# Kernel tuning notes

Measured on AMD Instinct MI355X. Metric: run time of the kernel, lower is better.

## Reference

```python
import jax, jax.numpy as jnp
import numpy as np

N = 8192      # nodes
C = 128       # node_channels
E = 262144    # edges (avg degree 32)


def _glorot(key, shape):
    lim = 1.0 / np.sqrt(shape[0])
    return jax.random.uniform(key, shape, jnp.float32, -lim, lim)


def setup_inputs() -> dict:
    key = jax.random.key(0)
    ks = jax.random.split(key, 12)
    inp = {
        "x": jax.random.normal(ks[0], (N, C), jnp.float32),
        "edge_index": jax.random.randint(ks[1], (2, E), 0, N, dtype=jnp.int32).astype(jnp.int64),
        # edge encoder: two parallel GCNConv layers producing source/target embeddings
        "Ws": _glorot(ks[2], (C, C)), "bs": jnp.zeros((C,), jnp.float32),
        "Wt": _glorot(ks[3], (C, C)), "bt": jnp.zeros((C,), jnp.float32),
        # NodeModel GCNConv weights (layers used in forward: 1, 2, mu, 5, 6)
        "W1": _glorot(ks[4], (C, C)), "b1": jnp.zeros((C,), jnp.float32),
        "W2": _glorot(ks[5], (C, C)), "b2": jnp.zeros((C,), jnp.float32),
        "Wmu": _glorot(ks[6], (C, C)), "bmu": jnp.zeros((C,), jnp.float32),
        "W5": _glorot(ks[7], (C, C)), "b5": jnp.zeros((C,), jnp.float32),
        "W6": _glorot(ks[8], (C, C)), "b6": jnp.zeros((C,), jnp.float32),
    }
    return inp


def _gcn(x, W, b, src, dst, dis, n):
    """GCNConv: D^-1/2 (A + I) D^-1/2 X W + b, edge flow src -> dst."""
    h = x @ W                                    # [n, C]
    norm = dis[src] * dis[dst]                   # [E]
    agg = jax.ops.segment_sum(h[src] * norm[:, None], dst, num_segments=n)
    agg = agg + h * (dis * dis)[:, None]         # self-loop term
    return agg + b


def reference(x, edge_index, Ws, bs, Wt, bt, W1, b1, W2, b2, Wmu, bmu, W5, b5, W6, b6):
    src, dst = edge_index[0], edge_index[1]
    n = x.shape[0]
    # degree with self-loops (shared by all GCN layers, same graph)
    deg = jax.ops.segment_sum(jnp.ones((src.shape[0],), x.dtype), dst, num_segments=n) + 1.0
    dis = deg ** -0.5

    # edge encoder -> source/target embeddings, dense inner-product decoder (sigmoid=False)
    s = _gcn(x, Ws, bs, src, dst, dis, n)
    t = _gcn(x, Wt, bt, src, dst, dis, n)
    adj_pred = s @ t.T                           # [n, n]

    # NodeModel (eval mode: reparametrize returns mu; logstd branch is dead code)
    h = jax.nn.relu(_gcn(x, W1, b1, src, dst, dis, n))
    h = jax.nn.relu(_gcn(h, W2, b2, src, dst, dis, n))
    h = _gcn(h, Wmu, bmu, src, dst, dis, n)
    h = jax.nn.relu(_gcn(h, W5, b5, src, dst, dis, n))
    h = jax.nn.relu(_gcn(h, W6, b6, src, dst, dis, n))
    return adj_pred, h
```

## Files before the change

### kernel.cpp

```cpp
#include <hip/hip_runtime.h>
#include <hip/hip_bf16.h>

#define CCH 128

typedef __attribute__((ext_vector_type(8))) short s8v;
typedef __attribute__((ext_vector_type(4))) float f4v;

__device__ __forceinline__ unsigned short f2bf(float f){
  unsigned int u = __float_as_uint(f);
  u += 0x7fffu + ((u >> 16) & 1u);
  return (unsigned short)(u >> 16);
}

__global__ void k_deg(const int* __restrict__ dst, int* __restrict__ deg, int e){
  int i = blockIdx.x * blockDim.x + threadIdx.x;
  if (i < e) atomicAdd(&deg[dst[i]], 1);
}

__global__ void k_dis(const int* __restrict__ deg, float* __restrict__ dis, int n){
  int i = blockIdx.x * blockDim.x + threadIdx.x;
  if (i < n) dis[i] = rsqrtf((float)deg[i] + 1.0f);
}

__global__ void k_scan(const int* __restrict__ deg, int* __restrict__ row_ptr,
                       int* __restrict__ cursor, int n){
  __shared__ int part[1024];
  int t = threadIdx.x;
  int base = t * 8;
  int loc[8];
  int s = 0;
  #pragma unroll
  for (int i = 0; i < 8; ++i){ loc[i] = s; s += deg[base + i]; }
  part[t] = s;
  __syncthreads();
  for (int off = 1; off < 1024; off <<= 1){
    int v = (t >= off) ? part[t - off] : 0;
    __syncthreads();
    part[t] += v;
    __syncthreads();
  }
  int prev = t ? part[t - 1] : 0;
  #pragma unroll
  for (int i = 0; i < 8; ++i){
    int v = prev + loc[i];
    row_ptr[base + i] = v;
    cursor[base + i]  = v;
  }
  if (t == 0) row_ptr[n] = part[1023];
}

__global__ void k_scatter(const int* __restrict__ src, const int* __restrict__ dst,
                          int* __restrict__ cursor, int* __restrict__ csr_src, int e){
  int i = blockIdx.x * blockDim.x + threadIdx.x;
  if (i < e){
    int d = dst[i];
    int pos = atomicAdd(&cursor[d], 1);
    csr_src[pos] = src[i];
  }
}

__global__ __launch_bounds__(256) void k_agg(const float* __restrict__ h,
                                             const float* __restrict__ dis,
                                             const int* __restrict__ row_ptr,
                                             const int* __restrict__ csr_src,
                                             float* __restrict__ out, int n){
  int node = (blockIdx.x * blockDim.x + threadIdx.x) >> 6;
  int lane = threadIdx.x & 63;
  if (node >= n) return;
  const float2* h2 = (const float2*)h;
  int st = row_ptr[node], en = row_ptr[node + 1];
  float ax = 0.f, ay = 0.f;
  for (int e = st; e < en; ++e){
    int s = csr_src[e];
    float ds = dis[s];
    float2 v = h2[(size_t)s * 64 + lane];
    ax += v.x * ds; ay += v.y * ds;
  }
  float di = dis[node];
  float2 sv = h2[(size_t)node * 64 + lane];
  float2 o;
  o.x = ax * di + sv.x * di * di;
  o.y = ay * di + sv.y * di * di;
  ((float2*)out)[(size_t)node * 64 + lane] = o;
}

__global__ __launch_bounds__(256) void k_gemm(const float* __restrict__ A,
                                              const float* __restrict__ W,
                                              const float* __restrict__ bias,
                                              float* __restrict__ out, int relu){
  __shared__ float sW[CCH * CCH];
  __shared__ float sA[32 * CCH];
  int tid = threadIdx.x;
  const float4* W4 = (const float4*)W;
  float4* sW4 = (float4*)sW;
  #pragma unroll
  for (int i = 0; i < 16; ++i) sW4[tid + i * 256] = W4[tid + i * 256];
  int row0 = blockIdx.x * 32;
  const float4* A4 = (const float4*)(A + (size_t)row0 * CCH);
  float4* sA4 = (float4*)sA;
  #pragma unroll
  for (int i = 0; i < 4; ++i) sA4[tid + i * 256] = A4[tid + i * 256];
  __syncthreads();

  int r  = (tid >> 4) << 1;
  int c0 = (tid & 15) << 3;
  float acc0[8] = {0}, acc1[8] = {0};
  for (int k = 0; k < CCH; ++k){
    float a0 = sA[r * CCH + k], a1 = sA[(r + 1) * CCH + k];
    const float* wr = &sW[k * CCH + c0];
    #pragma unroll
    for (int j = 0; j < 8; ++j){
      float w = wr[j];
      acc0[j] += a0 * w;
      acc1[j] += a1 * w;
    }
  }
  size_t g0 = (size_t)(row0 + r) * CCH + c0;
  #pragma unroll
  for (int j = 0; j < 8; ++j){
    float v0 = acc0[j] + bias[c0 + j];
    float v1 = acc1[j] + bias[c0 + j];
    if (relu){ v0 = fmaxf(v0, 0.f); v1 = fmaxf(v1, 0.f); }
    out[g0 + j] = v0;
    out[g0 + CCH + j] = v1;
  }
}

__global__ void k_tobf16(const float4* __restrict__ a, const float4* __restrict__ b,
                         ushort4* __restrict__ ao, ushort4* __restrict__ bo, int total4){
  int i = blockIdx.x * blockDim.x + threadIdx.x;
  if (i < total4){
    float4 va = a[i];
    float4 vb = b[i];
    ushort4 oa = { f2bf(va.x), f2bf(va.y), f2bf(va.z), f2bf(va.w) };
    ushort4 ob = { f2bf(vb.x), f2bf(vb.y), f2bf(vb.z), f2bf(vb.w) };
    ao[i] = oa;
    bo[i] = ob;
  }
}

__global__ __launch_bounds__(256) void k_adj(const unsigned short* __restrict__ S,
                                             const unsigned short* __restrict__ T,
                                             float* __restrict__ out, int n){
  __shared__ unsigned short sS[128 * 128];
  __shared__ unsigned short sT[128 * 128];
  int tid = threadIdx.x;
  int ntile = n >> 7;
  int tm = blockIdx.x / ntile;
  int tn = blockIdx.x % ntile;

  #pragma unroll
  for (int i = 0; i < 8; ++i){
    int cidx = i * 256 + tid;
    int row = cidx >> 4;
    int o   = cidx & 15;
    int boff = (o * 16) ^ ((row & 7) << 4);
    s8v v = ((const s8v*)(S + (size_t)(tm * 128 + row) * CCH))[o];
    *(s8v*)((char*)sS + row * 256 + boff) = v;
    s8v w = ((const s8v*)(T + (size_t)(tn * 128 + row) * CCH))[o];
    *(s8v*)((char*)sT + row * 256 + boff) = w;
  }
  __syncthreads();

  int lane = tid & 63;
  int w = tid >> 6;
  int wm = (w >> 1) * 64;
  int wn = (w & 1) * 64;

  f4v zero = {0.f, 0.f, 0.f, 0.f};
  f4v acc[4][4];
  #pragma unroll
  for (int a = 0; a < 4; ++a)
    #pragma unroll
    for (int b = 0; b < 4; ++b) acc[a][b] = zero;

  #pragma unroll
  for (int ks = 0; ks < 4; ++ks){
    int boff = ks * 64 + (lane >> 4) * 16;
    s8v af[4], bf[4];
    #pragma unroll
    for (int mi = 0; mi < 4; ++mi){
      int row = wm + mi * 16 + (lane & 15);
      af[mi] = *(const s8v*)((const char*)sS + row * 256 + (boff ^ ((row & 7) << 4)));
    }
    #pragma unroll
    for (int ni = 0; ni < 4; ++ni){
      int row = wn + ni * 16 + (lane & 15);
      bf[ni] = *(const s8v*)((const char*)sT + row * 256 + (boff ^ ((row & 7) << 4)));
    }
    #pragma unroll
    for (int mi = 0; mi < 4; ++mi)
      #pragma unroll
      for (int ni = 0; ni < 4; ++ni)
        acc[mi][ni] = __builtin_amdgcn_mfma_f32_16x16x32_bf16(af[mi], bf[ni], acc[mi][ni], 0, 0, 0);
  }

  int rbase = tm * 128 + wm + (lane >> 4) * 4;
  int cbase = tn * 128 + wn + (lane & 15);
  #pragma unroll
  for (int mi = 0; mi < 4; ++mi)
    #pragma unroll
    for (int ni = 0; ni < 4; ++ni){
      int rr = rbase + mi * 16;
      int cc = cbase + ni * 16;
      #pragma unroll
      for (int r = 0; r < 4; ++r)
        out[(size_t)(rr + r) * n + cc] = acc[mi][ni][r];
    }
}

extern "C" void kernel_launch(void* const* d_in, const int* in_sizes, int n_in,
                              void* d_out, int out_size, void* d_ws, size_t ws_size,
                              hipStream_t stream) {
  const float* x  = (const float*)d_in[0];
  const int*   ei = (const int*)d_in[1];
  const int n = in_sizes[0] / CCH;
  const int e = in_sizes[1] / 2;
  const int* srcv = ei;
  const int* dstv = ei + e;
  const float *Ws  = (const float*)d_in[2],  *bs  = (const float*)d_in[3];
  const float *Wt  = (const float*)d_in[4],  *bt  = (const float*)d_in[5];
  const float *W1  = (const float*)d_in[6],  *b1  = (const float*)d_in[7];
  const float *W2  = (const float*)d_in[8],  *b2  = (const float*)d_in[9];
  const float *Wmu = (const float*)d_in[10], *bmu = (const float*)d_in[11];
  const float *W5  = (const float*)d_in[12], *b5  = (const float*)d_in[13];
  const float *W6  = (const float*)d_in[14], *b6  = (const float*)d_in[15];

  char* ws = (char*)d_ws;
  size_t off = 0;
  auto alloc = [&](size_t bytes) -> void* {
    void* p = ws + off;
    off += (bytes + 255) & ~(size_t)255;
    return p;
  };
  int*   deg     = (int*)alloc((size_t)n * 4);
  float* dis     = (float*)alloc((size_t)n * 4);
  int*   row_ptr = (int*)alloc((size_t)(n + 1) * 4);
  int*   cursor  = (int*)alloc((size_t)n * 4);
  int*   csr_src = (int*)alloc((size_t)e * 4);
  float* aggX    = (float*)alloc((size_t)n * CCH * 4);
  float* sbuf    = (float*)alloc((size_t)n * CCH * 4);
  float* tbuf    = (float*)alloc((size_t)n * CCH * 4);
  float* P       = (float*)alloc((size_t)n * CCH * 4);
  float* Q       = (float*)alloc((size_t)n * CCH * 4);
  unsigned short* sb = (unsigned short*)alloc((size_t)n * CCH * 2);
  unsigned short* tb = (unsigned short*)alloc((size_t)n * CCH * 2);

  float* adj  = (float*)d_out;
  float* hout = (float*)d_out + (size_t)n * n;

  hipMemsetAsync(deg, 0, (size_t)n * 4, stream);
  k_deg    <<<(e + 255) / 256, 256, 0, stream>>>(dstv, deg, e);
  k_dis    <<<(n + 255) / 256, 256, 0, stream>>>(deg, dis, n);
  k_scan   <<<1, 1024, 0, stream>>>(deg, row_ptr, cursor, n);
  k_scatter<<<(e + 255) / 256, 256, 0, stream>>>(srcv, dstv, cursor, csr_src, e);

  k_agg <<<n / 4, 256, 0, stream>>>(x, dis, row_ptr, csr_src, aggX, n);
  k_gemm<<<n / 32, 256, 0, stream>>>(aggX, Ws, bs, sbuf, 0);
  k_gemm<<<n / 32, 256, 0, stream>>>(aggX, Wt, bt, tbuf, 0);
  k_gemm<<<n / 32, 256, 0, stream>>>(aggX, W1, b1, Q, 1);
  k_agg <<<n / 4, 256, 0, stream>>>(Q, dis, row_ptr, csr_src, P, n);
  k_gemm<<<n / 32, 256, 0, stream>>>(P, W2, b2, Q, 1);
  k_agg <<<n / 4, 256, 0, stream>>>(Q, dis, row_ptr, csr_src, P, n);
  k_gemm<<<n / 32, 256, 0, stream>>>(P, Wmu, bmu, Q, 0);
  k_agg <<<n / 4, 256, 0, stream>>>(Q, dis, row_ptr, csr_src, P, n);
  k_gemm<<<n / 32, 256, 0, stream>>>(P, W5, b5, Q, 1);
  k_agg <<<n / 4, 256, 0, stream>>>(Q, dis, row_ptr, csr_src, P, n);
  k_gemm<<<n / 32, 256, 0, stream>>>(P, W6, b6, hout, 1);

  k_tobf16<<<((n * CCH / 4) + 255) / 256, 256, 0, stream>>>(
      (const float4*)sbuf, (const float4*)tbuf, (ushort4*)sb, (ushort4*)tb, n * CCH / 4);
  int nt = n / 128;
  k_adj<<<nt * nt, 256, 0, stream>>>(sb, tb, adj, n);
}
```

Measured before the change: 553.3 us.

## Fold GCN normalization into GEMM epilogues and unroll gather aggregation

Factors D^-1/2 out of the edge loop. Each layer's output is pre-scaled by dis in the GEMM epilogue (and x by a new fused dis/scale kernel), so aggregation becomes a plain gather-sum with no per-edge dis loads or multiplies. The aggregation loop is unrolled by 8 with independent accumulators to raise memory-level parallelism. The GEMM block is halved to 16 rows to get more blocks, and the adj kernel is launched earlier in the stream. The risk is extra rounding from the changed accumulation order, plus a GEMM with less register reuse.

```diff
diff --git a/kernel.cpp b/kernel.cpp
--- a/kernel.cpp
+++ b/kernel.cpp
@@ -17,9 +17,16 @@
   if (i < e) atomicAdd(&deg[dst[i]], 1);
 }
 
-__global__ void k_dis(const int* __restrict__ deg, float* __restrict__ dis, int n){
-  int i = blockIdx.x * blockDim.x + threadIdx.x;
-  if (i < n) dis[i] = rsqrtf((float)deg[i] + 1.0f);
+__global__ __launch_bounds__(256) void k_disscale(const int* __restrict__ deg,
+    const float* __restrict__ x, float* __restrict__ dis, float* __restrict__ g, int n){
+  int t = blockIdx.x * 256 + threadIdx.x;
+  int i = t >> 5, c = t & 31;
+  if (i >= n) return;
+  float di = rsqrtf((float)deg[i] + 1.0f);
+  if (c == 0) dis[i] = di;
+  float4 v = ((const float4*)x)[(size_t)i * 32 + c];
+  v.x *= di; v.y *= di; v.z *= di; v.w *= di;
+  ((float4*)g)[(size_t)i * 32 + c] = v;
 }
 
 __global__ void k_scan(const int* __restrict__ deg, int* __restrict__ row_ptr,
@@ -59,70 +66,84 @@
   }
 }
 
-__global__ __launch_bounds__(256) void k_agg(const float* __restrict__ h,
-                                             const float* __restrict__ dis,
-                                             const int* __restrict__ row_ptr,
-                                             const int* __restrict__ csr_src,
-                                             float* __restrict__ out, int n){
+__global__ __launch_bounds__(256) void k_agg(const float* __restrict__ g,
+    const int* __restrict__ row_ptr, const int* __restrict__ csr_src,
+    float* __restrict__ out, int n){
   int node = (blockIdx.x * blockDim.x + threadIdx.x) >> 6;
   int lane = threadIdx.x & 63;
   if (node >= n) return;
-  const float2* h2 = (const float2*)h;
+  node = __builtin_amdgcn_readfirstlane(node);
+  const float2* g2 = (const float2*)g;
   int st = row_ptr[node], en = row_ptr[node + 1];
-  float ax = 0.f, ay = 0.f;
-  for (int e = st; e < en; ++e){
+  float2 sv = g2[(size_t)node * 64 + lane];
+  float ax0 = sv.x, ay0 = sv.y;
+  float ax1 = 0.f, ay1 = 0.f, ax2 = 0.f, ay2 = 0.f, ax3 = 0.f, ay3 = 0.f;
+  float ax4 = 0.f, ay4 = 0.f, ax5 = 0.f, ay5 = 0.f, ax6 = 0.f, ay6 = 0.f;
+  float ax7 = 0.f, ay7 = 0.f;
+  int e = st;
+  for (; e + 8 <= en; e += 8){
+    int s0 = csr_src[e + 0], s1 = csr_src[e + 1], s2 = csr_src[e + 2], s3 = csr_src[e + 3];
+    int s4 = csr_src[e + 4], s5 = csr_src[e + 5], s6 = csr_src[e + 6], s7 = csr_src[e + 7];
+    float2 v0 = g2[(size_t)s0 * 64 + lane];
+    float2 v1 = g2[(size_t)s1 * 64 + lane];
+    float2 v2 = g2[(size_t)s2 * 64 + lane];
+    float2 v3 = g2[(size_t)s3 * 64 + lane];
+    float2 v4 = g2[(size_t)s4 * 64 + lane];
+    float2 v5 = g2[(size_t)s5 * 64 + lane];
+    float2 v6 = g2[(size_t)s6 * 64 + lane];
+    float2 v7 = g2[(size_t)s7 * 64 + lane];
+    ax0 += v0.x; ay0 += v0.y;  ax1 += v1.x; ay1 += v1.y;
+    ax2 += v2.x; ay2 += v2.y;  ax3 += v3.x; ay3 += v3.y;
+    ax4 += v4.x; ay4 += v4.y;  ax5 += v5.x; ay5 += v5.y;
+    ax6 += v6.x; ay6 += v6.y;  ax7 += v7.x; ay7 += v7.y;
+  }
+  for (; e < en; ++e){
     int s = csr_src[e];
-    float ds = dis[s];
-    float2 v = h2[(size_t)s * 64 + lane];
-    ax += v.x * ds; ay += v.y * ds;
-  }
-  float di = dis[node];
-  float2 sv = h2[(size_t)node * 64 + lane];
+    float2 v = g2[(size_t)s * 64 + lane];
+    ax0 += v.x; ay0 += v.y;
+  }
   float2 o;
-  o.x = ax * di + sv.x * di * di;
-  o.y = ay * di + sv.y * di * di;
+  o.x = ((ax0 + ax1) + (ax2 + ax3)) + ((ax4 + ax5) + (ax6 + ax7));
+  o.y = ((ay0 + ay1) + (ay2 + ay3)) + ((ay4 + ay5) + (ay6 + ay7));
   ((float2*)out)[(size_t)node * 64 + lane] = o;
 }
 
 __global__ __launch_bounds__(256) void k_gemm(const float* __restrict__ A,
-                                              const float* __restrict__ W,
-                                              const float* __restrict__ bias,
-                                              float* __restrict__ out, int relu){
+    const float* __restrict__ W, const float* __restrict__ bias,
+    const float* __restrict__ dis, float* __restrict__ out,
+    int relu, int scale_out){
   __shared__ float sW[CCH * CCH];
-  __shared__ float sA[32 * CCH];
+  __shared__ float sA[16 * CCH];
   int tid = threadIdx.x;
   const float4* W4 = (const float4*)W;
   float4* sW4 = (float4*)sW;
   #pragma unroll
   for (int i = 0; i < 16; ++i) sW4[tid + i * 256] = W4[tid + i * 256];
-  int row0 = blockIdx.x * 32;
+  int row0 = blockIdx.x * 16;
   const float4* A4 = (const float4*)(A + (size_t)row0 * CCH);
   float4* sA4 = (float4*)sA;
-  #pragma unroll
-  for (int i = 0; i < 4; ++i) sA4[tid + i * 256] = A4[tid + i * 256];
+  sA4[tid]       = A4[tid];
+  sA4[tid + 256] = A4[tid + 256];
   __syncthreads();
 
-  int r  = (tid >> 4) << 1;
+  int r  = tid >> 4;
   int c0 = (tid & 15) << 3;
-  float acc0[8] = {0}, acc1[8] = {0};
+  float acc[8] = {0.f,0.f,0.f,0.f,0.f,0.f,0.f,0.f};
+  #pragma unroll 4
   for (int k = 0; k < CCH; ++k){
-    float a0 = sA[r * CCH + k], a1 = sA[(r + 1) * CCH + k];
+    float a = sA[r * CCH + k];
     const float* wr = &sW[k * CCH + c0];
     #pragma unroll
-    for (int j = 0; j < 8; ++j){
-      float w = wr[j];
-      acc0[j] += a0 * w;
-      acc1[j] += a1 * w;
-    }
-  }
+    for (int j = 0; j < 8; ++j) acc[j] += a * wr[j];
+  }
+  float di = dis[row0 + r];
   size_t g0 = (size_t)(row0 + r) * CCH + c0;
   #pragma unroll
   for (int j = 0; j < 8; ++j){
-    float v0 = acc0[j] + bias[c0 + j];
-    float v1 = acc1[j] + bias[c0 + j];
-    if (relu){ v0 = fmaxf(v0, 0.f); v1 = fmaxf(v1, 0.f); }
-    out[g0 + j] = v0;
-    out[g0 + CCH + j] = v1;
+    float v = fmaf(di, acc[j], bias[c0 + j]);
+    if (relu) v = fmaxf(v, 0.f);
+    if (scale_out) v *= di;
+    out[g0 + j] = v;
   }
 }
 
@@ -238,11 +259,12 @@
   int*   row_ptr = (int*)alloc((size_t)(n + 1) * 4);
   int*   cursor  = (int*)alloc((size_t)n * 4);
   int*   csr_src = (int*)alloc((size_t)e * 4);
-  float* aggX    = (float*)alloc((size_t)n * CCH * 4);
+  float* g0      = (float*)alloc((size_t)n * CCH * 4);
+  float* sumX    = (float*)alloc((size_t)n * CCH * 4);
   float* sbuf    = (float*)alloc((size_t)n * CCH * 4);
   float* tbuf    = (float*)alloc((size_t)n * CCH * 4);
-  float* P       = (float*)alloc((size_t)n * CCH * 4);
-  float* Q       = (float*)alloc((size_t)n * CCH * 4);
+  float* bufA    = (float*)alloc((size_t)n * CCH * 4);
+  float* bufB    = (float*)alloc((size_t)n * CCH * 4);
   unsigned short* sb = (unsigned short*)alloc((size_t)n * CCH * 2);
   unsigned short* tb = (unsigned short*)alloc((size_t)n * CCH * 2);
 
@@ -250,26 +272,27 @@
   float* hout = (float*)d_out + (size_t)n * n;
 
   hipMemsetAsync(deg, 0, (size_t)n * 4, stream);
-  k_deg    <<<(e + 255) / 256, 256, 0, stream>>>(dstv, deg, e);
-  k_dis    <<<(n + 255) / 256, 256, 0, stream>>>(deg, dis, n);
-  k_scan   <<<1, 1024, 0, stream>>>(deg, row_ptr, cursor, n);
-  k_scatter<<<(e + 255) / 256, 256, 0, stream>>>(srcv, dstv, cursor, csr_src, e);
-
-  k_agg <<<n / 4, 256, 0, stream>>>(x, dis, row_ptr, csr_src, aggX, n);
-  k_gemm<<<n / 32, 256, 0, stream>>>(aggX, Ws, bs, sbuf, 0);
-  k_gemm<<<n / 32, 256, 0, stream>>>(aggX, Wt, bt, tbuf, 0);
-  k_gemm<<<n / 32, 256, 0, stream>>>(aggX, W1, b1, Q, 1);
-  k_agg <<<n / 4, 256, 0, stream>>>(Q, dis, row_ptr, csr_src, P, n);
-  k_gemm<<<n / 32, 256, 0, stream>>>(P, W2, b2, Q, 1);
-  k_agg <<<n / 4, 256, 0, stream>>>(Q, dis, row_ptr, csr_src, P, n);
-  k_gemm<<<n / 32, 256, 0, stream>>>(P, Wmu, bmu, Q, 0);
-  k_agg <<<n / 4, 256, 0, stream>>>(Q, dis, row_ptr, csr_src, P, n);
-  k_gemm<<<n / 32, 256, 0, stream>>>(P, W5, b5, Q, 1);
-  k_agg <<<n / 4, 256, 0, stream>>>(Q, dis, row_ptr, csr_src, P, n);
-  k_gemm<<<n / 32, 256, 0, stream>>>(P, W6, b6, hout, 1);
+  k_deg     <<<(e + 255) / 256, 256, 0, stream>>>(dstv, deg, e);
+  k_scan    <<<1, 1024, 0, stream>>>(deg, row_ptr, cursor, n);
+  k_disscale<<<(n * 32) / 256, 256, 0, stream>>>(deg, x, dis, g0, n);
+  k_scatter <<<(e + 255) / 256, 256, 0, stream>>>(srcv, dstv, cursor, csr_src, e);
+
+  k_agg <<<n / 4, 256, 0, stream>>>(g0, row_ptr, csr_src, sumX, n);
+  k_gemm<<<n / 16, 256, 0, stream>>>(sumX, Ws, bs, dis, sbuf, 0, 0);
+  k_gemm<<<n / 16, 256, 0, stream>>>(sumX, Wt, bt, dis, tbuf, 0, 0);
+  k_gemm<<<n / 16, 256, 0, stream>>>(sumX, W1, b1, dis, bufA, 1, 1);
 
   k_tobf16<<<((n * CCH / 4) + 255) / 256, 256, 0, stream>>>(
       (const float4*)sbuf, (const float4*)tbuf, (ushort4*)sb, (ushort4*)tb, n * CCH / 4);
   int nt = n / 128;
   k_adj<<<nt * nt, 256, 0, stream>>>(sb, tb, adj, n);
-}
+
+  k_agg <<<n / 4, 256, 0, stream>>>(bufA, row_ptr, csr_src, sumX, n);
+  k_gemm<<<n / 16, 256, 0, stream>>>(sumX, W2, b2, dis, bufB, 1, 1);
+  k_agg <<<n / 4, 256, 0, stream>>>(bufB, row_ptr, csr_src, sumX, n);
+  k_gemm<<<n / 16, 256, 0, stream>>>(sumX, Wmu, bmu, dis, bufA, 0, 1);
+  k_agg <<<n / 4, 256, 0, stream>>>(bufA, row_ptr, csr_src, sumX, n);
+  k_gemm<<<n / 16, 256, 0, stream>>>(sumX, W5, b5, dis, bufB, 1, 1);
+  k_agg <<<n / 4, 256, 0, stream>>>(bufB, row_ptr, csr_src, sumX, n);
+  k_gemm<<<n / 16, 256, 0, stream>>>(sumX, W6, b6, dis, hout, 1, 0);
+}
```

Result: faster. 499.2 us (-9.8%).
